# Kernel optimization log

Hardware: AMD Instinct MI355X
Metric: run time of the kernel (lower is better)

Reference implementation:

```python
import jax, jax.numpy as jnp
import numpy as np

HEADS = 16
HEAD_DIM = 64
DIM = 1024
INNER = HEADS * HEAD_DIM
EPS = 1e-5


def setup_inputs() -> dict:
    key = jax.random.key(0)
    k_x, k_qkv, k_out, k_b = jax.random.split(key, 4)
    B, L = 2, 2048
    x = jax.random.normal(k_x, (B, L, DIM), dtype=jnp.float32)
    # Linear weights stored as [in, out] for x @ W
    w_qkv = jax.random.normal(k_qkv, (DIM, 3 * INNER), dtype=jnp.float32) * (DIM ** -0.5)
    w_out = jax.random.normal(k_out, (INNER, DIM), dtype=jnp.float32) * (INNER ** -0.5)
    b_out = jax.random.normal(k_b, (DIM,), dtype=jnp.float32) * 0.02
    gamma = jnp.ones((DIM,), dtype=jnp.float32)
    beta = jnp.zeros((DIM,), dtype=jnp.float32)
    return {"x": x, "w_qkv": w_qkv, "w_out": w_out, "b_out": b_out, "gamma": gamma, "beta": beta}


def reference(x, w_qkv, w_out, b_out, gamma, beta):
    B, L, C = x.shape
    scale = HEAD_DIM ** -0.5
    qkv = x @ w_qkv  # [B, L, 3*INNER]
    q, k, v = jnp.split(qkv, 3, axis=-1)
    # [B, L, INNER] -> [B, H, L, D]
    def split_heads(t):
        return t.reshape(B, L, HEADS, HEAD_DIM).transpose(0, 2, 1, 3)
    q, k, v = split_heads(q), split_heads(k), split_heads(v)
    dots = jnp.einsum('bhid,bhjd->bhij', q, k) * scale
    attn = jax.nn.softmax(dots, axis=-1)
    out = jnp.einsum('bhij,bhjd->bhid', attn, v)
    out = out.transpose(0, 2, 1, 3).reshape(B, L, INNER)
    out = out @ w_out + b_out
    res = x + out
    mean = jnp.mean(res, axis=-1, keepdims=True)
    var = jnp.var(res, axis=-1, keepdims=True)
    return (res - mean) * jax.lax.rsqrt(var + EPS) * gamma + beta
```

## Files before the change

kernel.cpp:

```cpp
#include <hip/hip_runtime.h>
#include <hip/hip_bf16.h>
#include <stdint.h>

#define HEADS 16
#define HDIM  64
#define DIMC  1024
#define INNER 1024
#define LSEQ  2048
#define BLM   4096

typedef unsigned short u16;
typedef __attribute__((ext_vector_type(8))) short bf16x8;
typedef __attribute__((ext_vector_type(4))) float f32x4;

__device__ __forceinline__ u16 f2bf(float f) {
  union { float f; uint32_t u; } v; v.f = f;
  uint32_t u = v.u;
  return (u16)((u + 0x7fffu + ((u >> 16) & 1u)) >> 16);
}
__device__ __forceinline__ uint32_t pack_bf2(float a, float b) {
  float2 f2; f2.x = a; f2.y = b;
  __hip_bfloat162 t = __float22bfloat162_rn(f2);
  union { __hip_bfloat162 h; uint32_t u; } c; c.h = t; return c.u;
}

__device__ __forceinline__ void load_lds16(const void* g, void* l) {
  __builtin_amdgcn_global_load_lds(
      (const __attribute__((address_space(1))) uint32_t*)g,
      (__attribute__((address_space(3))) uint32_t*)l, 16, 0, 0);
}

__global__ __launch_bounds__(256) void cast_bf16_k(const float* __restrict__ in,
                                                   u16* __restrict__ out, int n) {
  int i = (blockIdx.x * 256 + threadIdx.x) * 4;
  if (i < n) {
    float4 v = *(const float4*)(in + i);
    ushort4 o;
    o.x = f2bf(v.x); o.y = f2bf(v.y); o.z = f2bf(v.z); o.w = f2bf(v.w);
    *(ushort4*)(out + i) = o;
  }
}

__global__ __launch_bounds__(256) void transpose_cast_k(const float* __restrict__ in,
                                                        u16* __restrict__ out,
                                                        int R, int C) {
  __shared__ float tile[32][33];
  int c0 = blockIdx.x * 32, r0 = blockIdx.y * 32;
  int j = threadIdx.x & 31, i0 = threadIdx.x >> 5;
#pragma unroll
  for (int p = 0; p < 4; ++p) {
    int i = i0 + p * 8;
    tile[i][j] = in[(size_t)(r0 + i) * C + (c0 + j)];
  }
  __syncthreads();
#pragma unroll
  for (int p = 0; p < 4; ++p) {
    int i = i0 + p * 8;
    out[(size_t)(c0 + i) * R + (r0 + j)] = f2bf(tile[j][i]);
  }
}

template <int EPI>
__global__ __launch_bounds__(256) void gemm_bt(const u16* __restrict__ A,
                                               const u16* __restrict__ Bt,
                                               u16* __restrict__ Cb,
                                               float* __restrict__ Cf,
                                               const float* __restrict__ bias,
                                               const float* __restrict__ resid,
                                               u16* __restrict__ Vt,
                                               int M, int N, int K) {
  __shared__ alignas(16) u16 As[128 * 32];
  __shared__ alignas(16) u16 Bs[128 * 32];
  const int tid = threadIdx.x;
  const int lane = tid & 63;
  const int w = tid >> 6;
  const int wm = w >> 1, wn = w & 1;
  const int m0 = blockIdx.y * 128, n0 = blockIdx.x * 128;
  const int ln = lane & 15, qq = lane >> 4;
  const f32x4 zero4 = {0.f, 0.f, 0.f, 0.f};

  f32x4 acc[4][4];
#pragma unroll
  for (int i = 0; i < 4; ++i)
#pragma unroll
    for (int j = 0; j < 4; ++j) acc[i][j] = zero4;

  for (int kt = 0; kt < K; kt += 32) {
    __syncthreads();
#pragma unroll
    for (int iss = 0; iss < 2; ++iss) {
      int t = iss * 256 + tid;
      int r = t >> 2;
      int cl = (t & 3) ^ ((r >> 1) & 3);
      load_lds16(A + (size_t)(m0 + r) * K + kt + cl * 8,
                 (char*)As + (iss * 256 + w * 64) * 16);
      load_lds16(Bt + (size_t)(n0 + r) * K + kt + cl * 8,
                 (char*)Bs + (iss * 256 + w * 64) * 16);
    }
    __syncthreads();
    bf16x8 af[4], bfr[4];
#pragma unroll
    for (int i = 0; i < 4; ++i) {
      int ra = wm * 64 + i * 16 + ln;
      af[i] = *(const bf16x8*)(As + (ra * 4 + (qq ^ ((ra >> 1) & 3))) * 8);
      int rb = wn * 64 + i * 16 + ln;
      bfr[i] = *(const bf16x8*)(Bs + (rb * 4 + (qq ^ ((rb >> 1) & 3))) * 8);
    }
#pragma unroll
    for (int i = 0; i < 4; ++i)
#pragma unroll
      for (int j = 0; j < 4; ++j)
        acc[i][j] = __builtin_amdgcn_mfma_f32_16x16x32_bf16(af[i], bfr[j],
                                                            acc[i][j], 0, 0, 0);
  }

#pragma unroll
  for (int i = 0; i < 4; ++i) {
#pragma unroll
    for (int j = 0; j < 4; ++j) {
      int col = n0 + wn * 64 + j * 16 + ln;
      if (EPI == 0) {
#pragma unroll
        for (int rr = 0; rr < 4; ++rr) {
          int row = m0 + wm * 64 + i * 16 + qq * 4 + rr;
          Cb[(size_t)row * N + col] = f2bf(acc[i][j][rr]);
        }
      } else if (EPI == 1) {
#pragma unroll
        for (int rr = 0; rr < 4; ++rr) {
          int row = m0 + wm * 64 + i * 16 + qq * 4 + rr;
          Cf[(size_t)row * N + col] =
              acc[i][j][rr] + bias[col] + resid[(size_t)row * N + col];
        }
      } else {
        if (col < 2048) {
#pragma unroll
          for (int rr = 0; rr < 4; ++rr) {
            int row = m0 + wm * 64 + i * 16 + qq * 4 + rr;
            Cb[(size_t)row * 2048 + col] = f2bf(acc[i][j][rr]);
          }
        } else {
          int dg = col - 2048;
          int hh = dg >> 6, dd = dg & 63;
          int l0 = (m0 & 2047) + wm * 64 + i * 16 + qq * 4;
          int bb = m0 >> 11;
          ushort4 pk;
          pk.x = f2bf(acc[i][j][0]); pk.y = f2bf(acc[i][j][1]);
          pk.z = f2bf(acc[i][j][2]); pk.w = f2bf(acc[i][j][3]);
          *(ushort4*)(Vt + (((size_t)bb * 16 + hh) * 64 + dd) * 2048 + l0) = pk;
        }
      }
    }
  }
}

__global__ __launch_bounds__(256) void attn_fused(const u16* __restrict__ qk,
                                                  const u16* __restrict__ vt,
                                                  u16* __restrict__ outp) {
  const int qt = blockIdx.x & 15;
  const int h = (blockIdx.x >> 4) & 15;
  const int b = blockIdx.x >> 8;
  const int tid = threadIdx.x;
  const int lane = tid & 63;
  const int w = tid >> 6;
  const int ln = lane & 15, q4 = lane >> 4;
  const int l7 = ln & 7;
  const f32x4 zero4 = {0.f, 0.f, 0.f, 0.f};

  __shared__ alignas(16) u16 Ks[64 * 64];
  __shared__ alignas(16) u16 Vs[64 * 64];
  __shared__ alignas(16) u16 Ps[4][32 * 72];

  const size_t bh_tok = (size_t)b * LSEQ;
  const size_t vbase = ((size_t)b * 16 + h) * 64 * 2048;
  const int baseQ = h * HDIM;

  bf16x8 qf[2][2];
#pragma unroll
  for (int qi = 0; qi < 2; ++qi) {
    int row = qt * 128 + w * 32 + qi * 16 + ln;
    const u16* p = qk + (bh_tok + row) * 2048 + baseQ;
#pragma unroll
    for (int ks = 0; ks < 2; ++ks) {
      bf16x8 v = *(const bf16x8*)(p + q4 * 8 + 32 * ks);
      bf16x8 o;
#pragma unroll
      for (int jj = 0; jj < 8; ++jj) {
        union { uint32_t u; float f; } cv; cv.u = ((uint32_t)(u16)v[jj]) << 16;
        o[jj] = (short)f2bf(cv.f * 0.125f);
      }
      qf[ks][qi] = o;
    }
  }

  float mT[2] = {-1e30f, -1e30f}, lsum[2] = {0.f, 0.f};
  f32x4 o_acc[2][4];
#pragma unroll
  for (int qi = 0; qi < 2; ++qi)
#pragma unroll
    for (int dt = 0; dt < 4; ++dt) o_acc[qi][dt] = zero4;

  u16* pw_base = &Ps[w][0];

  for (int jt = 0; jt < 32; ++jt) {
    const int key0 = jt * 64;
    __syncthreads();
#pragma unroll
    for (int iss = 0; iss < 2; ++iss) {
      int idx = iss * 256 + tid;
      int row = idx >> 3, c = idx & 7;
      int cl = c ^ (row & 7);
      load_lds16(qk + (bh_tok + key0 + row) * 2048 + 1024 + baseQ + cl * 8,
                 (char*)Ks + (iss * 256 + w * 64) * 16);
      load_lds16(vt + vbase + (size_t)row * 2048 + key0 + cl * 8,
                 (char*)Vs + (iss * 256 + w * 64) * 16);
    }
    __syncthreads();

    f32x4 S2[2][4];
#pragma unroll
    for (int qi = 0; qi < 2; ++qi)
#pragma unroll
      for (int kt = 0; kt < 4; ++kt) S2[qi][kt] = zero4;
#pragma unroll
    for (int kt = 0; kt < 4; ++kt)
#pragma unroll
      for (int ks = 0; ks < 2; ++ks) {
        bf16x8 kf = *(const bf16x8*)(
            Ks + (((kt * 16 + ln) * 8 + ((ks * 4 + q4) ^ l7)) * 8));
#pragma unroll
        for (int qi = 0; qi < 2; ++qi)
          S2[qi][kt] = __builtin_amdgcn_mfma_f32_16x16x32_bf16(
              kf, qf[ks][qi], S2[qi][kt], 0, 0, 0);
      }

#pragma unroll
    for (int qi = 0; qi < 2; ++qi) {
      float mx = S2[qi][0][0];
#pragma unroll
      for (int kt = 0; kt < 4; ++kt)
#pragma unroll
        for (int r = 0; r < 4; ++r) mx = fmaxf(mx, S2[qi][kt][r]);
      mx = fmaxf(mx, __shfl_xor(mx, 16));
      mx = fmaxf(mx, __shfl_xor(mx, 32));
      float mnew = fmaxf(mT[qi], mx);
      float alpha = __expf(mT[qi] - mnew);
      float sl = 0.f;
#pragma unroll
      for (int kt = 0; kt < 4; ++kt)
#pragma unroll
        for (int r = 0; r < 4; ++r) {
          float p = __expf(S2[qi][kt][r] - mnew);
          S2[qi][kt][r] = p;
          sl += p;
        }
      sl += __shfl_xor(sl, 16);
      sl += __shfl_xor(sl, 32);
      lsum[qi] = lsum[qi] * alpha + sl;
      mT[qi] = mnew;
#pragma unroll
      for (int dt = 0; dt < 4; ++dt) o_acc[qi][dt] *= alpha;

#pragma unroll
      for (int kt = 0; kt < 4; ++kt) {
        uint2 pd;
        pd.x = pack_bf2(S2[qi][kt][0], S2[qi][kt][1]);
        pd.y = pack_bf2(S2[qi][kt][2], S2[qi][kt][3]);
        *(uint2*)(pw_base + (qi * 16 + ln) * 72 + kt * 16 + q4 * 4) = pd;
      }
    }
    asm volatile("s_waitcnt lgkmcnt(0)" ::: "memory");

    bf16x8 pf[2][2];
#pragma unroll
    for (int qi = 0; qi < 2; ++qi)
#pragma unroll
      for (int ks = 0; ks < 2; ++ks)
        pf[qi][ks] = *(const bf16x8*)(pw_base + (qi * 16 + ln) * 72 + ks * 32 +
                                      q4 * 8);

#pragma unroll
    for (int dt = 0; dt < 4; ++dt)
#pragma unroll
      for (int ks = 0; ks < 2; ++ks) {
        bf16x8 va = *(const bf16x8*)(
            Vs + (((dt * 16 + ln) * 8 + ((ks * 4 + q4) ^ l7)) * 8));
#pragma unroll
        for (int qi = 0; qi < 2; ++qi)
          o_acc[qi][dt] = __builtin_amdgcn_mfma_f32_16x16x32_bf16(
              va, pf[qi][ks], o_acc[qi][dt], 0, 0, 0);
      }
  }

  asm volatile("s_waitcnt lgkmcnt(0)" ::: "memory");
#pragma unroll
  for (int qi = 0; qi < 2; ++qi) {
    float rl = 1.0f / lsum[qi];
#pragma unroll
    for (int dt = 0; dt < 4; ++dt) {
      uint2 pd;
      pd.x = pack_bf2(o_acc[qi][dt][0] * rl, o_acc[qi][dt][1] * rl);
      pd.y = pack_bf2(o_acc[qi][dt][2] * rl, o_acc[qi][dt][3] * rl);
      *(uint2*)(pw_base + (qi * 16 + ln) * 72 + dt * 16 + q4 * 4) = pd;
    }
  }
  asm volatile("s_waitcnt lgkmcnt(0)" ::: "memory");
#pragma unroll
  for (int pass = 0; pass < 4; ++pass) {
    int rr = pass * 8 + (lane >> 3);
    int ch = lane & 7;
    bf16x8 rowv = *(const bf16x8*)(pw_base + rr * 72 + ch * 8);
    int tok = qt * 128 + w * 32 + rr;
    *(bf16x8*)(outp + (bh_tok + tok) * 1024 + baseQ + ch * 8) = rowv;
  }
}

__global__ __launch_bounds__(256) void ln_k(const float* __restrict__ res,
                                            const float* __restrict__ gamma,
                                            const float* __restrict__ beta,
                                            float* __restrict__ out) {
  int row = blockIdx.x;
  const float* r = res + (size_t)row * DIMC;
  int tid = threadIdx.x;
  float4 v = *(const float4*)(r + tid * 4);
  float s = v.x + v.y + v.z + v.w;
  float ss = v.x * v.x + v.y * v.y + v.z * v.z + v.w * v.w;
#pragma unroll
  for (int off = 1; off < 64; off <<= 1) {
    s += __shfl_xor(s, off);
    ss += __shfl_xor(ss, off);
  }
  __shared__ float sbuf[8];
  int w = tid >> 6, lane = tid & 63;
  if (lane == 0) { sbuf[w] = s; sbuf[4 + w] = ss; }
  __syncthreads();
  s = sbuf[0] + sbuf[1] + sbuf[2] + sbuf[3];
  ss = sbuf[4] + sbuf[5] + sbuf[6] + sbuf[7];
  float mean = s * (1.0f / DIMC);
  float var = ss * (1.0f / DIMC) - mean * mean;
  float inv = rsqrtf(var + 1e-5f);
  float4 g = *(const float4*)(gamma + tid * 4);
  float4 bt = *(const float4*)(beta + tid * 4);
  float4 o;
  o.x = (v.x - mean) * inv * g.x + bt.x;
  o.y = (v.y - mean) * inv * g.y + bt.y;
  o.z = (v.z - mean) * inv * g.z + bt.z;
  o.w = (v.w - mean) * inv * g.w + bt.w;
  *(float4*)(out + (size_t)row * DIMC + tid * 4) = o;
}

extern "C" void kernel_launch(void* const* d_in, const int* in_sizes, int n_in,
                              void* d_out, int out_size, void* d_ws, size_t ws_size,
                              hipStream_t stream) {
  const float* x = (const float*)d_in[0];
  const float* w_qkv = (const float*)d_in[1];
  const float* w_out = (const float*)d_in[2];
  const float* b_out = (const float*)d_in[3];
  const float* gamma = (const float*)d_in[4];
  const float* beta = (const float*)d_in[5];
  float* outp = (float*)d_out;
  char* ws = (char*)d_ws;

  u16* xb = (u16*)(ws);
  u16* wqkvT = (u16*)(ws + ((size_t)8 << 20));
  u16* qk = (u16*)(ws + ((size_t)14 << 20));
  u16* vt = (u16*)(ws + ((size_t)30 << 20));
  u16* attnout = (u16*)(ws);
  u16* woutT = (u16*)(ws + ((size_t)8 << 20));
  float* res = (float*)(ws + ((size_t)14 << 20));

  cast_bf16_k<<<4096, 256, 0, stream>>>(x, xb, BLM * DIMC);
  transpose_cast_k<<<dim3(96, 32), 256, 0, stream>>>(w_qkv, wqkvT, 1024, 3072);
  gemm_bt<2><<<dim3(24, 32), 256, 0, stream>>>(xb, wqkvT, qk, nullptr, nullptr,
                                               nullptr, vt, BLM, 3072, 1024);
  transpose_cast_k<<<dim3(32, 32), 256, 0, stream>>>(w_out, woutT, 1024, 1024);
  attn_fused<<<512, 256, 0, stream>>>(qk, vt, attnout);
  gemm_bt<1><<<dim3(8, 32), 256, 0, stream>>>(attnout, woutT, nullptr, res, b_out,
                                              x, nullptr, BLM, 1024, 1024);
  ln_k<<<4096, 256, 0, stream>>>(res, gamma, beta, outp);
}
```

Baseline: 235.9 us.

## Double-buffer K/V tiles in attention and switch softmax to exp2

The attention kernel now keeps two LDS buffers for K and V. It issues the global-to-LDS loads for the next key tile before computing on the current one, so only one barrier per iteration remains and memory latency can overlap the MFMA and softmax work. Q is also prescaled by log2(e) so the softmax can use exp2f instead of __expf, which saves a multiply per exponential. In exchange, LDS use per block rises, which may limit how many blocks fit on a CU.

```diff
diff --git a/kernel.cpp b/kernel.cpp
--- a/kernel.cpp
+++ b/kernel.cpp
@@ -167,14 +167,20 @@
   const int l7 = ln & 7;
   const f32x4 zero4 = {0.f, 0.f, 0.f, 0.f};
 
-  __shared__ alignas(16) u16 Ks[64 * 64];
-  __shared__ alignas(16) u16 Vs[64 * 64];
+  __shared__ alignas(16) u16 Ks[2][64 * 64];
+  __shared__ alignas(16) u16 Vs[2][64 * 64];
   __shared__ alignas(16) u16 Ps[4][32 * 72];
 
   const size_t bh_tok = (size_t)b * LSEQ;
   const size_t vbase = ((size_t)b * 16 + h) * 64 * 2048;
   const int baseQ = h * HDIM;
 
+  const int dma_row0 = tid >> 3, dma_c0 = tid & 7;
+  const int dma_cl0 = dma_c0 ^ (dma_row0 & 7);
+  const int dma_row1 = (256 + tid) >> 3, dma_c1 = tid & 7;
+  const int dma_cl1 = dma_c1 ^ (dma_row1 & 7);
+
+  const float qscale = 0.125f * 1.44269504088896340736f;
   bf16x8 qf[2][2];
 #pragma unroll
   for (int qi = 0; qi < 2; ++qi) {
@@ -187,7 +193,7 @@
 #pragma unroll
       for (int jj = 0; jj < 8; ++jj) {
         union { uint32_t u; float f; } cv; cv.u = ((uint32_t)(u16)v[jj]) << 16;
-        o[jj] = (short)f2bf(cv.f * 0.125f);
+        o[jj] = (short)f2bf(cv.f * qscale);
       }
       qf[ks][qi] = o;
     }
@@ -202,20 +208,37 @@
 
   u16* pw_base = &Ps[w][0];
 
+  {
+    const int key0 = 0;
+    load_lds16(qk + (bh_tok + key0 + dma_row0) * 2048 + 1024 + baseQ + dma_cl0 * 8,
+               (char*)Ks[0] + (w * 64) * 16);
+    load_lds16(vt + vbase + (size_t)dma_row0 * 2048 + key0 + dma_cl0 * 8,
+               (char*)Vs[0] + (w * 64) * 16);
+    load_lds16(qk + (bh_tok + key0 + dma_row1) * 2048 + 1024 + baseQ + dma_cl1 * 8,
+               (char*)Ks[0] + (256 + w * 64) * 16);
+    load_lds16(vt + vbase + (size_t)dma_row1 * 2048 + key0 + dma_cl1 * 8,
+               (char*)Vs[0] + (256 + w * 64) * 16);
+  }
+
   for (int jt = 0; jt < 32; ++jt) {
-    const int key0 = jt * 64;
+    const int cur = jt & 1;
     __syncthreads();
-#pragma unroll
-    for (int iss = 0; iss < 2; ++iss) {
-      int idx = iss * 256 + tid;
-      int row = idx >> 3, c = idx & 7;
-      int cl = c ^ (row & 7);
-      load_lds16(qk + (bh_tok + key0 + row) * 2048 + 1024 + baseQ + cl * 8,
-                 (char*)Ks + (iss * 256 + w * 64) * 16);
-      load_lds16(vt + vbase + (size_t)row * 2048 + key0 + cl * 8,
-                 (char*)Vs + (iss * 256 + w * 64) * 16);
-    }
-    __syncthreads();
+
+    if (jt + 1 < 32) {
+      const int nb = cur ^ 1;
+      const int key0 = (jt + 1) * 64;
+      load_lds16(qk + (bh_tok + key0 + dma_row0) * 2048 + 1024 + baseQ + dma_cl0 * 8,
+                 (char*)Ks[nb] + (w * 64) * 16);
+      load_lds16(vt + vbase + (size_t)dma_row0 * 2048 + key0 + dma_cl0 * 8,
+                 (char*)Vs[nb] + (w * 64) * 16);
+      load_lds16(qk + (bh_tok + key0 + dma_row1) * 2048 + 1024 + baseQ + dma_cl1 * 8,
+                 (char*)Ks[nb] + (256 + w * 64) * 16);
+      load_lds16(vt + vbase + (size_t)dma_row1 * 2048 + key0 + dma_cl1 * 8,
+                 (char*)Vs[nb] + (256 + w * 64) * 16);
+    }
+
+    const u16* Kc = Ks[cur];
+    const u16* Vc = Vs[cur];
 
     f32x4 S2[2][4];
 #pragma unroll
@@ -227,7 +250,7 @@
 #pragma unroll
       for (int ks = 0; ks < 2; ++ks) {
         bf16x8 kf = *(const bf16x8*)(
-            Ks + (((kt * 16 + ln) * 8 + ((ks * 4 + q4) ^ l7)) * 8));
+            Kc + (((kt * 16 + ln) * 8 + ((ks * 4 + q4) ^ l7)) * 8));
 #pragma unroll
         for (int qi = 0; qi < 2; ++qi)
           S2[qi][kt] = __builtin_amdgcn_mfma_f32_16x16x32_bf16(
@@ -244,13 +267,13 @@
       mx = fmaxf(mx, __shfl_xor(mx, 16));
       mx = fmaxf(mx, __shfl_xor(mx, 32));
       float mnew = fmaxf(mT[qi], mx);
-      float alpha = __expf(mT[qi] - mnew);
+      float alpha = exp2f(mT[qi] - mnew);
       float sl = 0.f;
 #pragma unroll
       for (int kt = 0; kt < 4; ++kt)
 #pragma unroll
         for (int r = 0; r < 4; ++r) {
-          float p = __expf(S2[qi][kt][r] - mnew);
+          float p = exp2f(S2[qi][kt][r] - mnew);
           S2[qi][kt][r] = p;
           sl += p;
         }
@@ -284,7 +307,7 @@
 #pragma unroll
       for (int ks = 0; ks < 2; ++ks) {
         bf16x8 va = *(const bf16x8*)(
-            Vs + (((dt * 16 + ln) * 8 + ((ks * 4 + q4) ^ l7)) * 8));
+            Vc + (((dt * 16 + ln) * 8 + ((ks * 4 + q4) ^ l7)) * 8));
 #pragma unroll
         for (int qi = 0; qi < 2; ++qi)
           o_acc[qi][dt] = __builtin_amdgcn_mfma_f32_16x16x32_bf16(
```

After: 251.2 us. 1.07x slower.
